# Optimization experiments

Hardware: AMD Instinct MI355X
Metric: run time of the kernel (lower is better)

The kernel has to match this reference:

```python
import jax, jax.numpy as jnp
import numpy as np

JET_FEATURES_WEIGHT = 1.0


def setup_inputs() -> dict:
    key = jax.random.key(0)
    k1, k2 = jax.random.split(key)
    B, N, D = 64, 2048, 4
    p = jax.random.normal(k1, (B, N, D), dtype=jnp.float32)
    q = jax.random.normal(k2, (B, N, D), dtype=jnp.float32)
    return {"p": p, "q": q}


def reference(p, q):
    # pairwise squared Euclidean (cartesian norm) distances via the
    # |p|^2 + |q|^2 - 2 p.q expansion (avoids a (B,N,N,4) broadcast temp)
    p_sq = jnp.sum(p * p, axis=-1)                      # (B, N)
    q_sq = jnp.sum(q * q, axis=-1)                      # (B, N)
    cross = jnp.einsum("bnd,bmd->bnm", p, q)            # (B, N, N)
    dist = p_sq[:, :, None] + q_sq[:, None, :] - 2.0 * cross  # (B, N, N)

    min_pq = jnp.min(dist, axis=-1)                     # (B, N) nearest q for each p
    min_qp = jnp.min(dist, axis=-2)                     # (B, N) nearest p for each q
    chamfer_loss = jnp.sum(min_pq + min_qp)

    # jet-level term: normsq of the difference of total 4-momenta
    jet_diff = jnp.sum(p, axis=-2) - jnp.sum(q, axis=-2)  # (B, 4)
    jet_loss = jnp.sum(jet_diff * jet_diff)

    return chamfer_loss + JET_FEATURES_WEIGHT * jet_loss
```

## Files before the change

### kernel.cpp

```cpp
#include <hip/hip_runtime.h>

#define N_PTS  2048
#define BATCH  64
#define NSLICE 32
#define SLICE  (N_PTS / NSLICE)
#define P      8
#define BLK    256

static_assert(P * BLK == N_PTS, "block must cover all rows for col-final mins");
static_assert(SLICE <= BLK, "one staged point per thread");

__device__ __forceinline__ int fkey(float v) {
    int b = __float_as_int(v);
    return b >= 0 ? b : b ^ 0x7fffffff;
}
__device__ __forceinline__ float funkey(int b) {
    return __int_as_float(b >= 0 ? b : b ^ 0x7fffffff);
}

template <bool ATOMIC>
__global__ __launch_bounds__(BLK, 4) void chamfer_partial(
        const float4* __restrict__ p,
        const float4* __restrict__ q,
        float* __restrict__ wrow,
        float* __restrict__ wcol,
        float* __restrict__ out) {
    __shared__ float4 sQ[SLICE];
    __shared__ float4 sQs4[SLICE / 4];
    __shared__ int    colk[SLICE];

    const int tid = threadIdx.x;
    const int s   = blockIdx.x;
    const int b   = blockIdx.y;
    const float4* __restrict__ Pb = p + (size_t)b * N_PTS;
    const float4* __restrict__ Qb = q + (size_t)b * N_PTS + s * SLICE;

    if (s == 0 && b == 0 && tid == 0) out[0] = 0.0f;

    if (tid < SLICE) {
        const float4 v = Qb[tid];
        sQ[tid] = v;
        ((float*)sQs4)[tid] = v.x * v.x + v.y * v.y + v.z * v.z + v.w * v.w;
        colk[tid] = 0x7FFFFFFF;
    }
    __syncthreads();

    float4 pm[P];
    float  psq[P];
    float  mn[P];
#pragma unroll
    for (int k = 0; k < P; ++k) {
        const float4 pv = Pb[tid + k * BLK];
        psq[k] = pv.x * pv.x + pv.y * pv.y + pv.z * pv.z + pv.w * pv.w;
        pm[k]  = make_float4(-2.0f * pv.x, -2.0f * pv.y, -2.0f * pv.z, -2.0f * pv.w);
        mn[k]  = 3.4e38f;
    }

#pragma unroll 1
    for (int j = 0; j < SLICE; j += 4) {
        const float4 qs = sQs4[j >> 2];
        const float4 q0 = sQ[j + 0];
        const float4 q1 = sQ[j + 1];
        const float4 q2 = sQ[j + 2];
        const float4 q3 = sQ[j + 3];
        float c0 = 3.4e38f, c1 = 3.4e38f, c2 = 3.4e38f, c3 = 3.4e38f;
#pragma unroll
        for (int k = 0; k < P; k += 2) {
            const float4 a0 = pm[k], a1 = pm[k + 1];
            const float  e0 = psq[k], e1 = psq[k + 1];
            float u00 = fmaf(a0.x, q0.x, qs.x + e0);
            u00 = fmaf(a0.y, q0.y, u00); u00 = fmaf(a0.z, q0.z, u00); u00 = fmaf(a0.w, q0.w, u00);
            float u01 = fmaf(a0.x, q1.x, qs.y + e0);
            u01 = fmaf(a0.y, q1.y, u01); u01 = fmaf(a0.z, q1.z, u01); u01 = fmaf(a0.w, q1.w, u01);
            float u02 = fmaf(a0.x, q2.x, qs.z + e0);
            u02 = fmaf(a0.y, q2.y, u02); u02 = fmaf(a0.z, q2.z, u02); u02 = fmaf(a0.w, q2.w, u02);
            float u03 = fmaf(a0.x, q3.x, qs.w + e0);
            u03 = fmaf(a0.y, q3.y, u03); u03 = fmaf(a0.z, q3.z, u03); u03 = fmaf(a0.w, q3.w, u03);
            float u10 = fmaf(a1.x, q0.x, qs.x + e1);
            u10 = fmaf(a1.y, q0.y, u10); u10 = fmaf(a1.z, q0.z, u10); u10 = fmaf(a1.w, q0.w, u10);
            float u11 = fmaf(a1.x, q1.x, qs.y + e1);
            u11 = fmaf(a1.y, q1.y, u11); u11 = fmaf(a1.z, q1.z, u11); u11 = fmaf(a1.w, q1.w, u11);
            float u12 = fmaf(a1.x, q2.x, qs.z + e1);
            u12 = fmaf(a1.y, q2.y, u12); u12 = fmaf(a1.z, q2.z, u12); u12 = fmaf(a1.w, q2.w, u12);
            float u13 = fmaf(a1.x, q3.x, qs.w + e1);
            u13 = fmaf(a1.y, q3.y, u13); u13 = fmaf(a1.z, q3.z, u13); u13 = fmaf(a1.w, q3.w, u13);
            asm("v_min3_f32 %0, %0, %1, %2" : "+v"(mn[k])     : "v"(u00), "v"(u01));
            asm("v_min3_f32 %0, %0, %1, %2" : "+v"(mn[k])     : "v"(u02), "v"(u03));
            asm("v_min3_f32 %0, %0, %1, %2" : "+v"(mn[k + 1]) : "v"(u10), "v"(u11));
            asm("v_min3_f32 %0, %0, %1, %2" : "+v"(mn[k + 1]) : "v"(u12), "v"(u13));
            asm("v_min3_f32 %0, %0, %1, %2" : "+v"(c0) : "v"(u00), "v"(u10));
            asm("v_min3_f32 %0, %0, %1, %2" : "+v"(c1) : "v"(u01), "v"(u11));
            asm("v_min3_f32 %0, %0, %1, %2" : "+v"(c2) : "v"(u02), "v"(u12));
            asm("v_min3_f32 %0, %0, %1, %2" : "+v"(c3) : "v"(u03), "v"(u13));
        }
        const int l = tid & 63;
        const float sa = (l & 1) ? c0 : c1;
        const float sb = (l & 1) ? c2 : c3;
        const float ka = (l & 1) ? c1 : c0;
        const float kb = (l & 1) ? c3 : c2;
        const float r0 = fminf(ka, __shfl_xor(sa, 1, 64));
        const float r1 = fminf(kb, __shfl_xor(sb, 1, 64));
        const float sc = (l & 2) ? r0 : r1;
        const float kc = (l & 2) ? r1 : r0;
        float m = fminf(kc, __shfl_xor(sc, 2, 64));
        m = fminf(m, __shfl_xor(m, 4, 64));
        m = fminf(m, __shfl_xor(m, 8, 64));
        m = fminf(m, __shfl_xor(m, 16, 64));
        if ((l & 31) < 4) atomicMin(&colk[j + (l & 3)], fkey(m));
    }

    if (ATOMIC) {
        int* wi = (int*)wrow + (size_t)b * N_PTS;
#pragma unroll
        for (int k = 0; k < P; ++k)
            atomicMin(wi + tid + k * BLK, fkey(mn[k]));
    } else {
        float* wf = wrow + ((size_t)b * NSLICE + s) * N_PTS;
#pragma unroll
        for (int k = 0; k < P; ++k)
            wf[tid + k * BLK] = mn[k];
    }

    __syncthreads();
    if (tid < SLICE)
        wcol[(size_t)b * N_PTS + s * SLICE + tid] = funkey(colk[tid]);
}

template <bool ATOMIC>
__global__ __launch_bounds__(256) void chamfer_finish(
        const float4* __restrict__ p,
        const float4* __restrict__ q,
        const float* __restrict__ wrow,
        const float* __restrict__ wcol,
        float* __restrict__ out) {
    __shared__ float wred[4];
    __shared__ float4 wacc[4];
    const int tid  = threadIdx.x;
    const int qi4  = blockIdx.x * 256 + tid;
    const int b    = blockIdx.y;
    const int lane = tid & 63;
    const int wid  = tid >> 6;

    float acc;
    if (ATOMIC) {
        const int4 v = ((const int4*)wrow)[(size_t)b * (N_PTS / 4) + qi4];
        acc = funkey(v.x) + funkey(v.y) + funkey(v.z) + funkey(v.w);
    } else {
        const float4* wf = (const float4*)wrow + (size_t)b * NSLICE * (N_PTS / 4);
        float4 m = wf[qi4];
#pragma unroll
        for (int s2 = 1; s2 < NSLICE; ++s2) {
            const float4 v = wf[(size_t)s2 * (N_PTS / 4) + qi4];
            m.x = fminf(m.x, v.x); m.y = fminf(m.y, v.y);
            m.z = fminf(m.z, v.z); m.w = fminf(m.w, v.w);
        }
        acc = (m.x + m.y) + (m.z + m.w);
    }
    {
        const float4 cv = ((const float4*)wcol)[(size_t)b * (N_PTS / 4) + qi4];
        acc += (cv.x + cv.y) + (cv.z + cv.w);
    }

#pragma unroll
    for (int off = 32; off > 0; off >>= 1) acc += __shfl_down(acc, off, 64);
    if (lane == 0) wred[wid] = acc;
    __syncthreads();
    if (tid == 0) {
        atomicAdd(out, wred[0] + wred[1] + wred[2] + wred[3]);
    }

    if (blockIdx.x == 0) {
        const float4* __restrict__ Pb = p + (size_t)b * N_PTS;
        const float4* __restrict__ Qb = q + (size_t)b * N_PTS;
        float ax = 0.f, ay = 0.f, az = 0.f, aw = 0.f;
        for (int j = tid; j < N_PTS; j += 256) {
            const float4 pv = Pb[j];
            const float4 qv = Qb[j];
            ax += pv.x - qv.x;
            ay += pv.y - qv.y;
            az += pv.z - qv.z;
            aw += pv.w - qv.w;
        }
#pragma unroll
        for (int off = 32; off > 0; off >>= 1) {
            ax += __shfl_down(ax, off, 64);
            ay += __shfl_down(ay, off, 64);
            az += __shfl_down(az, off, 64);
            aw += __shfl_down(aw, off, 64);
        }
        if (lane == 0) wacc[wid] = make_float4(ax, ay, az, aw);
        __syncthreads();
        if (tid == 0) {
            float dx = 0.f, dy = 0.f, dz = 0.f, dw = 0.f;
#pragma unroll
            for (int w = 0; w < 4; ++w) {
                dx += wacc[w].x; dy += wacc[w].y; dz += wacc[w].z; dw += wacc[w].w;
            }
            atomicAdd(out, dx * dx + dy * dy + dz * dz + dw * dw);
        }
    }
}

extern "C" void kernel_launch(void* const* d_in, const int* in_sizes, int n_in,
                              void* d_out, int out_size, void* d_ws, size_t ws_size,
                              hipStream_t stream) {
    const float4* p = (const float4*)d_in[0];
    const float4* q = (const float4*)d_in[1];
    float* out = (float*)d_out;
    float* ws  = (float*)d_ws;

    const size_t row_plain  = (size_t)BATCH * NSLICE * N_PTS;
    const size_t row_atomic = (size_t)BATCH * N_PTS;
    const size_t col_elems  = (size_t)BATCH * N_PTS;

    if (ws_size >= (row_plain + col_elems) * sizeof(float)) {
        float* wrow = ws;
        float* wcol = ws + row_plain;
        chamfer_partial<false><<<dim3(NSLICE, BATCH), BLK, 0, stream>>>(p, q, wrow, wcol, out);
        chamfer_finish<false><<<dim3(2, BATCH), 256, 0, stream>>>(p, q, wrow, wcol, out);
    } else {
        float* wrow = ws;
        float* wcol = ws + row_atomic;
        hipMemsetAsync(wrow, 0x7F, row_atomic * sizeof(int), stream);
        chamfer_partial<true><<<dim3(NSLICE, BATCH), BLK, 0, stream>>>(p, q, wrow, wcol, out);
        chamfer_finish<true><<<dim3(2, BATCH), 256, 0, stream>>>(p, q, wrow, wcol, out);
    }
}
```

Before: 105.8 us.

## Batch column-min reduction over 8 columns and split finish reduction across slices

The partial kernel now computes column minima for 8 q points per iteration and reduces them with a three-stage transpose-style shuffle tree, so every lane ends holding one column and issues an LDS atomicMin. This replaces per-4-column reductions that used 6 shuffles and atomics from only 8 lanes. The finish kernel launches 8 blocks per batch instead of 2, and each wave reduces 8 of the 32 slices before combining through shared memory. This spreads the slice-min reads over more threads. In exchange, register pressure rises and there are more LDS atomics per iteration and more global atomicAdds into the output.

```diff
diff --git a/kernel.cpp b/kernel.cpp
--- a/kernel.cpp
+++ b/kernel.cpp
@@ -56,57 +56,85 @@
         mn[k]  = 3.4e38f;
     }
 
+    const int l = tid & 63;
+
 #pragma unroll 1
-    for (int j = 0; j < SLICE; j += 4) {
-        const float4 qs = sQs4[j >> 2];
-        const float4 q0 = sQ[j + 0];
-        const float4 q1 = sQ[j + 1];
-        const float4 q2 = sQ[j + 2];
-        const float4 q3 = sQ[j + 3];
-        float c0 = 3.4e38f, c1 = 3.4e38f, c2 = 3.4e38f, c3 = 3.4e38f;
-#pragma unroll
-        for (int k = 0; k < P; k += 2) {
-            const float4 a0 = pm[k], a1 = pm[k + 1];
-            const float  e0 = psq[k], e1 = psq[k + 1];
-            float u00 = fmaf(a0.x, q0.x, qs.x + e0);
-            u00 = fmaf(a0.y, q0.y, u00); u00 = fmaf(a0.z, q0.z, u00); u00 = fmaf(a0.w, q0.w, u00);
-            float u01 = fmaf(a0.x, q1.x, qs.y + e0);
-            u01 = fmaf(a0.y, q1.y, u01); u01 = fmaf(a0.z, q1.z, u01); u01 = fmaf(a0.w, q1.w, u01);
-            float u02 = fmaf(a0.x, q2.x, qs.z + e0);
-            u02 = fmaf(a0.y, q2.y, u02); u02 = fmaf(a0.z, q2.z, u02); u02 = fmaf(a0.w, q2.w, u02);
-            float u03 = fmaf(a0.x, q3.x, qs.w + e0);
-            u03 = fmaf(a0.y, q3.y, u03); u03 = fmaf(a0.z, q3.z, u03); u03 = fmaf(a0.w, q3.w, u03);
-            float u10 = fmaf(a1.x, q0.x, qs.x + e1);
-            u10 = fmaf(a1.y, q0.y, u10); u10 = fmaf(a1.z, q0.z, u10); u10 = fmaf(a1.w, q0.w, u10);
-            float u11 = fmaf(a1.x, q1.x, qs.y + e1);
-            u11 = fmaf(a1.y, q1.y, u11); u11 = fmaf(a1.z, q1.z, u11); u11 = fmaf(a1.w, q1.w, u11);
-            float u12 = fmaf(a1.x, q2.x, qs.z + e1);
-            u12 = fmaf(a1.y, q2.y, u12); u12 = fmaf(a1.z, q2.z, u12); u12 = fmaf(a1.w, q2.w, u12);
-            float u13 = fmaf(a1.x, q3.x, qs.w + e1);
-            u13 = fmaf(a1.y, q3.y, u13); u13 = fmaf(a1.z, q3.z, u13); u13 = fmaf(a1.w, q3.w, u13);
-            asm("v_min3_f32 %0, %0, %1, %2" : "+v"(mn[k])     : "v"(u00), "v"(u01));
-            asm("v_min3_f32 %0, %0, %1, %2" : "+v"(mn[k])     : "v"(u02), "v"(u03));
-            asm("v_min3_f32 %0, %0, %1, %2" : "+v"(mn[k + 1]) : "v"(u10), "v"(u11));
-            asm("v_min3_f32 %0, %0, %1, %2" : "+v"(mn[k + 1]) : "v"(u12), "v"(u13));
-            asm("v_min3_f32 %0, %0, %1, %2" : "+v"(c0) : "v"(u00), "v"(u10));
-            asm("v_min3_f32 %0, %0, %1, %2" : "+v"(c1) : "v"(u01), "v"(u11));
-            asm("v_min3_f32 %0, %0, %1, %2" : "+v"(c2) : "v"(u02), "v"(u12));
-            asm("v_min3_f32 %0, %0, %1, %2" : "+v"(c3) : "v"(u03), "v"(u13));
-        }
-        const int l = tid & 63;
-        const float sa = (l & 1) ? c0 : c1;
-        const float sb = (l & 1) ? c2 : c3;
-        const float ka = (l & 1) ? c1 : c0;
-        const float kb = (l & 1) ? c3 : c2;
-        const float r0 = fminf(ka, __shfl_xor(sa, 1, 64));
-        const float r1 = fminf(kb, __shfl_xor(sb, 1, 64));
-        const float sc = (l & 2) ? r0 : r1;
-        const float kc = (l & 2) ? r1 : r0;
-        float m = fminf(kc, __shfl_xor(sc, 2, 64));
-        m = fminf(m, __shfl_xor(m, 4, 64));
-        m = fminf(m, __shfl_xor(m, 8, 64));
-        m = fminf(m, __shfl_xor(m, 16, 64));
-        if ((l & 31) < 4) atomicMin(&colk[j + (l & 3)], fkey(m));
+    for (int jj = 0; jj < SLICE; jj += 8) {
+        float c[8];
+#pragma unroll
+        for (int i = 0; i < 8; ++i) c[i] = 3.4e38f;
+
+#pragma unroll
+        for (int h = 0; h < 2; ++h) {
+            const int j = jj + 4 * h;
+            const float4 qs = sQs4[j >> 2];
+            const float4 q0 = sQ[j + 0];
+            const float4 q1 = sQ[j + 1];
+            const float4 q2 = sQ[j + 2];
+            const float4 q3 = sQ[j + 3];
+#pragma unroll
+            for (int k = 0; k < P; k += 2) {
+                const float4 a0 = pm[k], a1 = pm[k + 1];
+                const float  e0 = psq[k], e1 = psq[k + 1];
+                float u00 = fmaf(a0.x, q0.x, qs.x + e0);
+                u00 = fmaf(a0.y, q0.y, u00); u00 = fmaf(a0.z, q0.z, u00); u00 = fmaf(a0.w, q0.w, u00);
+                float u01 = fmaf(a0.x, q1.x, qs.y + e0);
+                u01 = fmaf(a0.y, q1.y, u01); u01 = fmaf(a0.z, q1.z, u01); u01 = fmaf(a0.w, q1.w, u01);
+                float u02 = fmaf(a0.x, q2.x, qs.z + e0);
+                u02 = fmaf(a0.y, q2.y, u02); u02 = fmaf(a0.z, q2.z, u02); u02 = fmaf(a0.w, q2.w, u02);
+                float u03 = fmaf(a0.x, q3.x, qs.w + e0);
+                u03 = fmaf(a0.y, q3.y, u03); u03 = fmaf(a0.z, q3.z, u03); u03 = fmaf(a0.w, q3.w, u03);
+                float u10 = fmaf(a1.x, q0.x, qs.x + e1);
+                u10 = fmaf(a1.y, q0.y, u10); u10 = fmaf(a1.z, q0.z, u10); u10 = fmaf(a1.w, q0.w, u10);
+                float u11 = fmaf(a1.x, q1.x, qs.y + e1);
+                u11 = fmaf(a1.y, q1.y, u11); u11 = fmaf(a1.z, q1.z, u11); u11 = fmaf(a1.w, q1.w, u11);
+                float u12 = fmaf(a1.x, q2.x, qs.z + e1);
+                u12 = fmaf(a1.y, q2.y, u12); u12 = fmaf(a1.z, q2.z, u12); u12 = fmaf(a1.w, q2.w, u12);
+                float u13 = fmaf(a1.x, q3.x, qs.w + e1);
+                u13 = fmaf(a1.y, q3.y, u13); u13 = fmaf(a1.z, q3.z, u13); u13 = fmaf(a1.w, q3.w, u13);
+                asm("v_min3_f32 %0, %0, %1, %2" : "+v"(mn[k])     : "v"(u00), "v"(u01));
+                asm("v_min3_f32 %0, %0, %1, %2" : "+v"(mn[k])     : "v"(u02), "v"(u03));
+                asm("v_min3_f32 %0, %0, %1, %2" : "+v"(mn[k + 1]) : "v"(u10), "v"(u11));
+                asm("v_min3_f32 %0, %0, %1, %2" : "+v"(mn[k + 1]) : "v"(u12), "v"(u13));
+                asm("v_min3_f32 %0, %0, %1, %2" : "+v"(c[4 * h + 0]) : "v"(u00), "v"(u10));
+                asm("v_min3_f32 %0, %0, %1, %2" : "+v"(c[4 * h + 1]) : "v"(u01), "v"(u11));
+                asm("v_min3_f32 %0, %0, %1, %2" : "+v"(c[4 * h + 2]) : "v"(u02), "v"(u12));
+                asm("v_min3_f32 %0, %0, %1, %2" : "+v"(c[4 * h + 3]) : "v"(u03), "v"(u13));
+            }
+        }
+
+        float r0, r1, r2, r3, t0, t1, m;
+        {
+            const bool b0 = (l & 1);
+            const float s0 = b0 ? c[0] : c[1];
+            const float s1 = b0 ? c[2] : c[3];
+            const float s2 = b0 ? c[4] : c[5];
+            const float s3 = b0 ? c[6] : c[7];
+            const float k0 = b0 ? c[1] : c[0];
+            const float k1 = b0 ? c[3] : c[2];
+            const float k2 = b0 ? c[5] : c[4];
+            const float k3 = b0 ? c[7] : c[6];
+            r0 = fminf(k0, __shfl_xor(s0, 1, 64));
+            r1 = fminf(k1, __shfl_xor(s1, 1, 64));
+            r2 = fminf(k2, __shfl_xor(s2, 1, 64));
+            r3 = fminf(k3, __shfl_xor(s3, 1, 64));
+        }
+        {
+            const bool b1 = (l & 2);
+            const float s0 = b1 ? r0 : r1;
+            const float s1 = b1 ? r2 : r3;
+            const float k0 = b1 ? r1 : r0;
+            const float k1 = b1 ? r3 : r2;
+            t0 = fminf(k0, __shfl_xor(s0, 2, 64));
+            t1 = fminf(k1, __shfl_xor(s1, 2, 64));
+        }
+        {
+            const bool b2 = (l & 4);
+            const float s0 = b2 ? t0 : t1;
+            const float k0 = b2 ? t1 : t0;
+            m = fminf(k0, __shfl_xor(s0, 4, 64));
+        }
+        atomicMin(&colk[jj + (l & 7)], fkey(m));
     }
 
     if (ATOMIC) {
@@ -133,40 +161,48 @@
         const float* __restrict__ wrow,
         const float* __restrict__ wcol,
         float* __restrict__ out) {
-    __shared__ float wred[4];
+    __shared__ float4 sm[4][64];
     __shared__ float4 wacc[4];
     const int tid  = threadIdx.x;
-    const int qi4  = blockIdx.x * 256 + tid;
+    const int l64  = tid & 63;
+    const int grp  = tid >> 6;
+    const int qi4  = blockIdx.x * 64 + l64;
     const int b    = blockIdx.y;
-    const int lane = tid & 63;
-    const int wid  = tid >> 6;
-
-    float acc;
+
     if (ATOMIC) {
-        const int4 v = ((const int4*)wrow)[(size_t)b * (N_PTS / 4) + qi4];
-        acc = funkey(v.x) + funkey(v.y) + funkey(v.z) + funkey(v.w);
+        if (grp == 0) {
+            const int4 v = ((const int4*)wrow)[(size_t)b * (N_PTS / 4) + qi4];
+            float acc = funkey(v.x) + funkey(v.y) + funkey(v.z) + funkey(v.w);
+            const float4 cv = ((const float4*)wcol)[(size_t)b * (N_PTS / 4) + qi4];
+            acc += (cv.x + cv.y) + (cv.z + cv.w);
+#pragma unroll
+            for (int off = 32; off > 0; off >>= 1) acc += __shfl_down(acc, off, 64);
+            if (l64 == 0) atomicAdd(out, acc);
+        }
     } else {
         const float4* wf = (const float4*)wrow + (size_t)b * NSLICE * (N_PTS / 4);
-        float4 m = wf[qi4];
-#pragma unroll
-        for (int s2 = 1; s2 < NSLICE; ++s2) {
-            const float4 v = wf[(size_t)s2 * (N_PTS / 4) + qi4];
+        float4 m = wf[(size_t)(grp * 8) * (N_PTS / 4) + qi4];
+#pragma unroll
+        for (int s2 = 1; s2 < 8; ++s2) {
+            const float4 v = wf[(size_t)(grp * 8 + s2) * (N_PTS / 4) + qi4];
             m.x = fminf(m.x, v.x); m.y = fminf(m.y, v.y);
             m.z = fminf(m.z, v.z); m.w = fminf(m.w, v.w);
         }
-        acc = (m.x + m.y) + (m.z + m.w);
-    }
-    {
-        const float4 cv = ((const float4*)wcol)[(size_t)b * (N_PTS / 4) + qi4];
-        acc += (cv.x + cv.y) + (cv.z + cv.w);
-    }
-
-#pragma unroll
-    for (int off = 32; off > 0; off >>= 1) acc += __shfl_down(acc, off, 64);
-    if (lane == 0) wred[wid] = acc;
-    __syncthreads();
-    if (tid == 0) {
-        atomicAdd(out, wred[0] + wred[1] + wred[2] + wred[3]);
+        sm[grp][l64] = m;
+        __syncthreads();
+        if (grp == 0) {
+            const float4 m1 = sm[1][l64], m2 = sm[2][l64], m3 = sm[3][l64];
+            m.x = fminf(fminf(m.x, m1.x), fminf(m2.x, m3.x));
+            m.y = fminf(fminf(m.y, m1.y), fminf(m2.y, m3.y));
+            m.z = fminf(fminf(m.z, m1.z), fminf(m2.z, m3.z));
+            m.w = fminf(fminf(m.w, m1.w), fminf(m2.w, m3.w));
+            float acc = (m.x + m.y) + (m.z + m.w);
+            const float4 cv = ((const float4*)wcol)[(size_t)b * (N_PTS / 4) + qi4];
+            acc += (cv.x + cv.y) + (cv.z + cv.w);
+#pragma unroll
+            for (int off = 32; off > 0; off >>= 1) acc += __shfl_down(acc, off, 64);
+            if (l64 == 0) atomicAdd(out, acc);
+        }
     }
 
     if (blockIdx.x == 0) {
@@ -188,7 +224,7 @@
             az += __shfl_down(az, off, 64);
             aw += __shfl_down(aw, off, 64);
         }
-        if (lane == 0) wacc[wid] = make_float4(ax, ay, az, aw);
+        if (l64 == 0) wacc[grp] = make_float4(ax, ay, az, aw);
         __syncthreads();
         if (tid == 0) {
             float dx = 0.f, dy = 0.f, dz = 0.f, dw = 0.f;
@@ -217,12 +253,12 @@
         float* wrow = ws;
         float* wcol = ws + row_plain;
         chamfer_partial<false><<<dim3(NSLICE, BATCH), BLK, 0, stream>>>(p, q, wrow, wcol, out);
-        chamfer_finish<false><<<dim3(2, BATCH), 256, 0, stream>>>(p, q, wrow, wcol, out);
+        chamfer_finish<false><<<dim3(8, BATCH), 256, 0, stream>>>(p, q, wrow, wcol, out);
     } else {
         float* wrow = ws;
         float* wcol = ws + row_atomic;
         hipMemsetAsync(wrow, 0x7F, row_atomic * sizeof(int), stream);
         chamfer_partial<true><<<dim3(NSLICE, BATCH), BLK, 0, stream>>>(p, q, wrow, wcol, out);
-        chamfer_finish<true><<<dim3(2, BATCH), 256, 0, stream>>>(p, q, wrow, wcol, out);
-    }
-}
+        chamfer_finish<true><<<dim3(8, BATCH), 256, 0, stream>>>(p, q, wrow, wcol, out);
+    }
+}
```

Result: slower. 109.8 us (+3.8%).
